# Performance work log

Hardware: AMD Instinct MI355X
Metric: run time of the kernel (lower is better)

Reference implementation:

```python
import jax, jax.numpy as jnp
import numpy as np

N = 4096      # n_patches / nodes
IN_FEAT = 512
EMBED = 512
HEADS = 8
HEAD_DIM = EMBED // HEADS
SCALING = HEAD_DIM ** -0.5


def setup_inputs() -> dict:
    key = jax.random.key(0)
    ks = jax.random.split(key, 7)
    x = jax.random.normal(ks[0], (N, IN_FEAT), dtype=jnp.float32)
    adj = jax.random.randint(ks[1], (N, N), 0, 2, dtype=jnp.int32)
    s = 0.04  # ~xavier scale for 512x512
    WQ = jax.random.normal(ks[2], (EMBED, IN_FEAT), dtype=jnp.float32) * s
    WK = jax.random.normal(ks[3], (EMBED, IN_FEAT), dtype=jnp.float32) * s
    WV = jax.random.normal(ks[4], (EMBED, IN_FEAT), dtype=jnp.float32) * s
    we = jax.random.normal(ks[5], (1, HEAD_DIM), dtype=jnp.float32) * 0.1
    be = jnp.zeros((1,), dtype=jnp.float32)
    return {"x": x, "adj": adj, "WQ": WQ, "WK": WK, "WV": WV, "we": we, "be": be}


def reference(x, adj, WQ, WK, WV, we, be):
    n = x.shape[0]
    # projections: [N, E] -> [H, N, head_dim]
    Q = (x @ WQ.T).reshape(n, HEADS, HEAD_DIM).transpose(1, 0, 2)
    K = (x @ WK.T).reshape(n, HEADS, HEAD_DIM).transpose(1, 0, 2)
    V = (x @ WV.T).reshape(n, HEADS, HEAD_DIM).transpose(1, 0, 2)
    # scores + per-query energy term: [H, N, N]
    energy = Q @ we.T + be                      # [H, N, 1]
    attn = jnp.einsum('hqd,hkd->hqk', Q, K) * SCALING + energy
    # adjacency mask (broadcast over heads)
    attn = attn + jnp.where(adj > 0, 0.0, -jnp.inf)
    attn = jax.nn.softmax(attn, axis=-1)
    # winner-take-all: one-hot at row max, divided by num_heads
    hard = (attn == jnp.max(attn, axis=-1, keepdims=True)).astype(jnp.float32) / HEADS
    out = jnp.einsum('hqk,hkd->hqd', hard, V)   # [H, N, head_dim]
    return out.transpose(1, 0, 2).reshape(n, EMBED)
```

## Files before the change

### kernel.cpp

```cpp
#include <hip/hip_runtime.h>
#include <hip/hip_bf16.h>
#include <float.h>
#include <stdint.h>

#define NPT    4096
#define EMB    512
#define NH     8
#define HD     64
#define KSPLIT 32

typedef __attribute__((ext_vector_type(8))) short bf16x8;
typedef __attribute__((ext_vector_type(4))) float f32x4;
typedef uint32_t u32;

__device__ __forceinline__ void async_ld16(const void* gsrc, void* ldst) {
    __builtin_amdgcn_global_load_lds(
        (const __attribute__((address_space(1))) u32*)gsrc,
        (__attribute__((address_space(3))) u32*)ldst, 16, 0, 0);
}

__device__ __forceinline__ void split3(float a, unsigned short& h,
                                       unsigned short& m, unsigned short& l) {
    __hip_bfloat16 bh = __float2bfloat16(a);
    float fh = __bfloat162float(bh);
    float r1 = a - fh;
    __hip_bfloat16 bm = __float2bfloat16(r1);
    float fm = __bfloat162float(bm);
    float r2 = r1 - fm;
    __hip_bfloat16 bl = __float2bfloat16(r2);
    h = *reinterpret_cast<unsigned short*>(&bh);
    m = *reinterpret_cast<unsigned short*>(&bm);
    l = *reinterpret_cast<unsigned short*>(&bl);
}

__global__ __launch_bounds__(256) void prep_kernel(const float* __restrict__ x,
                                                   const float* __restrict__ wq,
                                                   const float* __restrict__ wk,
                                                   const float* __restrict__ wv,
                                                   const int* __restrict__ adj,
                                                   unsigned short* __restrict__ xs,
                                                   unsigned short* __restrict__ wqs,
                                                   unsigned short* __restrict__ wks,
                                                   unsigned short* __restrict__ wvs,
                                                   unsigned* __restrict__ bits_t) {
    int y = blockIdx.y;
    size_t i = (size_t)blockIdx.x * 256 + threadIdx.x;
    if (y == 4) {
        int q = (int)(i >> 7), w = (int)i & 127;
        const int4* p = (const int4*)(adj + (size_t)q * NPT + w * 32);
        unsigned m = 0;
#pragma unroll
        for (int j = 0; j < 8; ++j) {
            int4 v = p[j];
            m |= (v.x != 0 ? 1u : 0u) << (j * 4 + 0);
            m |= (v.y != 0 ? 1u : 0u) << (j * 4 + 1);
            m |= (v.z != 0 ? 1u : 0u) << (j * 4 + 2);
            m |= (v.w != 0 ? 1u : 0u) << (j * 4 + 3);
        }
        bits_t[(size_t)w * NPT + q] = m;
    } else if (y == 0) {
        const size_t PL = (size_t)NPT * EMB;
        float4 v = ((const float4*)x)[i];
        ushort4 h, m, l;
        split3(v.x, h.x, m.x, l.x);
        split3(v.y, h.y, m.y, l.y);
        split3(v.z, h.z, m.z, l.z);
        split3(v.w, h.w, m.w, l.w);
        ((ushort4*)xs)[i]            = h;
        ((ushort4*)(xs + PL))[i]     = m;
        ((ushort4*)(xs + 2 * PL))[i] = l;
    } else {
        const size_t WPL = 262144;
        if (i >= WPL / 4) return;
        const float* src = (y == 1) ? wq : (y == 2) ? wk : wv;
        unsigned short* dst = (y == 1) ? wqs : (y == 2) ? wks : wvs;
        float4 v = ((const float4*)src)[i];
        int e  = (int)(i >> 7);
        int k0 = ((int)i & 127) * 4;
        int ebk = e >> 6, el = e & 63;
        int kc = k0 >> 5, g = (k0 >> 3) & 3, dd = k0 & 7;
        size_t off = ((((size_t)ebk * 16 + kc) * 4 + g) * 64 + el) * 8 + dd;
        ushort4 h, m, l;
        split3(v.x, h.x, m.x, l.x);
        split3(v.y, h.y, m.y, l.y);
        split3(v.z, h.z, m.z, l.z);
        split3(v.w, h.w, m.w, l.w);
        *(ushort4*)(dst + off)           = h;
        *(ushort4*)(dst + WPL + off)     = m;
        *(ushort4*)(dst + 2 * WPL + off) = l;
    }
}

__global__ __launch_bounds__(256) void gemm_mfma(const unsigned short* __restrict__ xs,
                                                 const unsigned short* __restrict__ wqs,
                                                 const unsigned short* __restrict__ wks,
                                                 const unsigned short* __restrict__ wvs,
                                                 unsigned short* __restrict__ Q3,
                                                 unsigned short* __restrict__ K3,
                                                 float* __restrict__ V) {
    const int z = blockIdx.z;
    const unsigned short* W3 = (z == 0) ? wqs : (z == 1) ? wks : wvs;
    const size_t XPL = (size_t)NPT * EMB;
    const size_t WPL = 262144;
    const size_t OPL = (size_t)NH * NPT * HD;

    const int nb = blockIdx.x * 128;
    const int ebk = blockIdx.y;
    const int tid = threadIdx.x;
    const int wv = tid >> 6, lane = tid & 63;
    const int m = lane & 15, quad = lane >> 4;
    const int n0 = nb + wv * 32;

    __shared__ __align__(16) unsigned short Ws[2][3 * 2048];

    auto prefetchW = [&](int kc, int buf) {
#pragma unroll
        for (int i2 = 0; i2 < 3; ++i2) {
            int c = wv + 4 * i2;
            int p = c >> 2, sub = c & 3;
            const unsigned short* src = W3 + (size_t)p * WPL
                + ((size_t)ebk * 16 + kc) * 2048 + (sub * 64 + lane) * 8;
            async_ld16(src, &Ws[buf][p * 2048 + sub * 512]);
        }
    };
    bf16x8 bfA[2][3], bfB[2][3];
    auto load_bf = [&](bf16x8 (&bf)[2][3], int kc) {
#pragma unroll
        for (int nt = 0; nt < 2; ++nt)
#pragma unroll
            for (int p = 0; p < 3; ++p)
                bf[nt][p] = *(const bf16x8*)(xs + (size_t)p * XPL
                    + (size_t)(n0 + nt * 16 + m) * EMB + kc * 32 + quad * 8);
    };

    f32x4 acc[4][2];
#pragma unroll
    for (int mt = 0; mt < 4; ++mt)
#pragma unroll
        for (int nt = 0; nt < 2; ++nt) acc[mt][nt] = (f32x4){0.f, 0.f, 0.f, 0.f};

    prefetchW(0, 0);
    load_bf(bfA, 0);

    auto iter = [&](int kc, int buf, bf16x8 (&cur)[2][3], bf16x8 (&nxt)[2][3]) {
        __syncthreads();
        if (kc < 15) { prefetchW(kc + 1, buf ^ 1); load_bf(nxt, kc + 1); }
#pragma unroll
        for (int ga = 0; ga < 3; ++ga) {
            bf16x8 af[4];
#pragma unroll
            for (int mt = 0; mt < 4; ++mt)
                af[mt] = *(const bf16x8*)&Ws[buf][ga * 2048 + (quad * 64 + mt * 16 + m) * 8];
#pragma unroll
            for (int pb = 0; pb < 3 - ga; ++pb)
#pragma unroll
                for (int mt = 0; mt < 4; ++mt)
#pragma unroll
                    for (int nt = 0; nt < 2; ++nt)
                        acc[mt][nt] = __builtin_amdgcn_mfma_f32_16x16x32_bf16(
                            af[mt], cur[nt][pb], acc[mt][nt], 0, 0, 0);
        }
    };

#pragma unroll 1
    for (int kc2 = 0; kc2 < 16; kc2 += 2) {
        iter(kc2, 0, bfA, bfB);
        iter(kc2 + 1, 1, bfB, bfA);
    }

    const int h = ebk;
#pragma unroll
    for (int mt = 0; mt < 4; ++mt)
#pragma unroll
        for (int nt = 0; nt < 2; ++nt) {
            const int n = n0 + nt * 16 + m;
            const int d0 = mt * 16 + quad * 4;
            f32x4 a = acc[mt][nt];
            if (z == 2) {
                *(f32x4*)(V + (size_t)n * EMB + ebk * 64 + d0) = a;
            } else {
                ushort4 ph, pm, pl;
                split3(a[0], ph.x, pm.x, pl.x);
                split3(a[1], ph.y, pm.y, pl.y);
                split3(a[2], ph.z, pm.z, pl.z);
                split3(a[3], ph.w, pm.w, pl.w);
                unsigned short* O3 = (z == 0) ? Q3 : K3;
                size_t off = ((size_t)h * 128 + (n >> 5)) * 2048
                           + (d0 >> 3) * 256 + (n & 31) * 8 + (d0 & 7);
                *(ushort4*)(O3 + off)           = ph;
                *(ushort4*)(O3 + OPL + off)     = pm;
                *(ushort4*)(O3 + 2 * OPL + off) = pl;
            }
        }
}

__global__ __launch_bounds__(256) void score_mfma(const unsigned short* __restrict__ Q3,
                                                  const unsigned short* __restrict__ K3,
                                                  const unsigned* __restrict__ bits_t,
                                                  float* __restrict__ pval,
                                                  int* __restrict__ pidx) {
    const int qb = blockIdx.x * 128;
    const int ks = blockIdx.y;
    const int tid = threadIdx.x;
    const int wv = tid >> 6, lane = tid & 63;
    const int m = lane & 15, quad = lane >> 4;
    const size_t PL = (size_t)NH * NPT * HD;
    const int kq = qb + wv * 32;

    __shared__ __align__(16) unsigned short Ks[3][3 * 2048];

    auto prefetchK = [&](int t) {
        int h = t >> 2, kt = ks * 4 + (t & 3), buf = t % 3;
#pragma unroll
        for (int i2 = 0; i2 < 3; ++i2) {
            int c = wv + 4 * i2;
            int p = c >> 2, sub = c & 3;
            const unsigned short* src = K3 + (size_t)p * PL
                + ((size_t)h * 128 + kt) * 2048 + (sub * 64 + lane) * 8;
            async_ld16(src, &Ks[buf][p * 2048 + sub * 512]);
        }
    };

    prefetchK(0);
    prefetchK(1);

    bf16x8 qf[2][2][3];
    float bestv[2]; int besti[2];

#pragma unroll 1
    for (int t = 0; t < NH * 4; ++t) {
        const int h = t >> 2, kst = t & 3, buf = t % 3;
        const int kbase = ks * 128 + kst * 32;

        asm volatile("s_waitcnt vmcnt(3)\n\ts_barrier" ::: "memory");

        if (kst == 0) {
#pragma unroll
            for (int nt = 0; nt < 2; ++nt)
#pragma unroll
                for (int dc = 0; dc < 2; ++dc)
#pragma unroll
                    for (int p = 0; p < 3; ++p)
                        qf[nt][dc][p] = *(const bf16x8*)(Q3 + (size_t)p * PL
                            + ((size_t)h * 128 + (kq >> 5)) * 2048
                            + (dc * 4 + quad) * 256 + (nt * 16 + m) * 8);
            bestv[0] = bestv[1] = -FLT_MAX;
            besti[0] = besti[1] = 0;
        }

        unsigned bw[2];
#pragma unroll
        for (int nt = 0; nt < 2; ++nt)
            bw[nt] = bits_t[(size_t)(ks * 4 + kst) * NPT + kq + nt * 16 + m];

        if (t + 2 < NH * 4) prefetchK(t + 2);

        f32x4 acc[2][2];
#pragma unroll
        for (int mt = 0; mt < 2; ++mt)
#pragma unroll
            for (int nt = 0; nt < 2; ++nt) acc[mt][nt] = (f32x4){0.f, 0.f, 0.f, 0.f};

#pragma unroll
        for (int ga = 0; ga < 3; ++ga) {
            bf16x8 kf[2][2];
#pragma unroll
            for (int mt = 0; mt < 2; ++mt)
#pragma unroll
                for (int dc = 0; dc < 2; ++dc)
                    kf[mt][dc] = *(const bf16x8*)
                        &Ks[buf][ga * 2048 + ((dc * 4 + quad) * 32 + mt * 16 + m) * 8];
#pragma unroll
            for (int pb = 0; pb < 3 - ga; ++pb)
#pragma unroll
                for (int dc = 0; dc < 2; ++dc)
#pragma unroll
                    for (int mt = 0; mt < 2; ++mt)
#pragma unroll
                        for (int nt = 0; nt < 2; ++nt)
                            acc[mt][nt] = __builtin_amdgcn_mfma_f32_16x16x32_bf16(
                                kf[mt][dc], qf[nt][dc][pb], acc[mt][nt], 0, 0, 0);
        }

#pragma unroll
        for (int nt = 0; nt < 2; ++nt) {
            unsigned w = bw[nt];
#pragma unroll
            for (int mt = 0; mt < 2; ++mt) {
                int k0 = mt * 16 + quad * 4;
                f32x4 a = acc[mt][nt];
#pragma unroll
                for (int r = 0; r < 4; ++r) {
                    if ((w >> (k0 + r)) & 1u) {
                        float s = a[r];
                        if (s > bestv[nt]) { bestv[nt] = s; besti[nt] = kbase + k0 + r; }
                    }
                }
            }
        }

        if (kst == 3) {
#pragma unroll
            for (int nt = 0; nt < 2; ++nt) {
                float v = bestv[nt]; int bi = besti[nt];
#pragma unroll
                for (int off = 16; off < 64; off <<= 1) {
                    float ov = __shfl_xor(v, off);
                    int   oi = __shfl_xor(bi, off);
                    if (ov > v || (ov == v && oi < bi)) { v = ov; bi = oi; }
                }
                if (quad == 0) {
                    size_t o = ((size_t)h * KSPLIT + ks) * NPT + kq + nt * 16 + m;
                    pval[o] = v; pidx[o] = bi;
                }
            }
        }
    }
}

__global__ __launch_bounds__(128) void gather_out(const float* __restrict__ V,
                                                  const float* __restrict__ pval,
                                                  const int* __restrict__ pidx,
                                                  float* __restrict__ out) {
    const int q = blockIdx.x;
    const int tid = threadIdx.x;
    __shared__ int widx[NH];
    if (tid < NH) {
        float bv = -FLT_MAX; int bi = 0;
        for (int ks = 0; ks < KSPLIT; ++ks) {
            size_t off = ((size_t)tid * KSPLIT + ks) * NPT + q;
            float v = pval[off];
            if (v > bv) { bv = v; bi = pidx[off]; }
        }
        widx[tid] = bi;
    }
    __syncthreads();
    const int h = tid >> 4;
    const int d4 = (tid & 15) * 4;
    const int k = widx[h];
    float4 v = *(const float4*)(V + (size_t)k * EMB + h * HD + d4);
    v.x *= 0.125f; v.y *= 0.125f; v.z *= 0.125f; v.w *= 0.125f;
    *(float4*)(out + (size_t)q * EMB + h * HD + d4) = v;
}

extern "C" void kernel_launch(void* const* d_in, const int* in_sizes, int n_in,
                              void* d_out, int out_size, void* d_ws, size_t ws_size,
                              hipStream_t stream) {
    const float* x   = (const float*)d_in[0];
    const int*   adj = (const int*)d_in[1];
    const float* WQ  = (const float*)d_in[2];
    const float* WK  = (const float*)d_in[3];
    const float* WV  = (const float*)d_in[4];
    float* out = (float*)d_out;

    char* ws = (char*)d_ws;
    const size_t HMB = 512u * 1024;
    unsigned short* xs   = (unsigned short*)(ws);
    unsigned short* wqs  = (unsigned short*)(ws + 24 * HMB);
    unsigned short* wks  = (unsigned short*)(ws + 27 * HMB);
    unsigned short* wvs  = (unsigned short*)(ws + 30 * HMB);
    unsigned short* Q3   = (unsigned short*)(ws + 33 * HMB);
    unsigned short* K3   = (unsigned short*)(ws + 57 * HMB);
    float*          V    = (float*)(ws + 81 * HMB);
    unsigned*       bits = (unsigned*)(ws + 97 * HMB);
    float*          pval = (float*)(ws);
    int*            pidx = (int*)(ws + 8 * HMB);

    prep_kernel<<<dim3(2048, 5), dim3(256), 0, stream>>>(x, WQ, WK, WV, adj,
                                                         xs, wqs, wks, wvs, bits);
    gemm_mfma<<<dim3(NPT / 128, NH, 3), dim3(256), 0, stream>>>(xs, wqs, wks, wvs, Q3, K3, V);
    score_mfma<<<dim3(NPT / 128, KSPLIT), dim3(256), 0, stream>>>(Q3, K3, bits, pval, pidx);
    gather_out<<<dim3(NPT), dim3(128), 0, stream>>>(V, pval, pidx, out);
}
```

Measured before the change: 276.2 us.

## Fuse Q/K/V projections into one GEMM block with tiled x layout

The projection GEMM now computes Q, K and V in a single block, so each loaded x fragment is reused across all three weight matrices instead of being reloaded by three separate z-blocks. The prep kernel writes x in a tiled 16-row by 32-column layout so the GEMM's fragment loads become contiguous. Warps are arranged 2x2 over n and e, and the grid shrinks from 768 to 256 blocks. The double-buffered prefetch is dropped in favour of a single buffer with two barriers per k-step, which exposes load latency and leaves fewer blocks per CU, while the 24 accumulator tiles per thread raise register pressure.

```diff
diff --git a/kernel.cpp b/kernel.cpp
--- a/kernel.cpp
+++ b/kernel.cpp
@@ -61,14 +61,18 @@
     } else if (y == 0) {
         const size_t PL = (size_t)NPT * EMB;
         float4 v = ((const float4*)x)[i];
+        int n  = (int)(i >> 7);
+        int k0 = ((int)i & 127) * 4;
+        int kc = k0 >> 5, kg = (k0 >> 3) & 3, dd = k0 & 7;
+        size_t off = ((((size_t)(n >> 4) * 16 + kc) * 4 + kg) * 16 + (n & 15)) * 8 + dd;
         ushort4 h, m, l;
         split3(v.x, h.x, m.x, l.x);
         split3(v.y, h.y, m.y, l.y);
         split3(v.z, h.z, m.z, l.z);
         split3(v.w, h.w, m.w, l.w);
-        ((ushort4*)xs)[i]            = h;
-        ((ushort4*)(xs + PL))[i]     = m;
-        ((ushort4*)(xs + 2 * PL))[i] = l;
+        *(ushort4*)(xs + off)          = h;
+        *(ushort4*)(xs + PL + off)     = m;
+        *(ushort4*)(xs + 2 * PL + off) = l;
     } else {
         const size_t WPL = 262144;
         if (i >= WPL / 4) return;
@@ -98,100 +102,100 @@
                                                  unsigned short* __restrict__ Q3,
                                                  unsigned short* __restrict__ K3,
                                                  float* __restrict__ V) {
-    const int z = blockIdx.z;
-    const unsigned short* W3 = (z == 0) ? wqs : (z == 1) ? wks : wvs;
     const size_t XPL = (size_t)NPT * EMB;
     const size_t WPL = 262144;
     const size_t OPL = (size_t)NH * NPT * HD;
 
-    const int nb = blockIdx.x * 128;
+    const int tn  = blockIdx.x;
     const int ebk = blockIdx.y;
     const int tid = threadIdx.x;
     const int wv = tid >> 6, lane = tid & 63;
+    const int wn = wv & 1, we = wv >> 1;
     const int m = lane & 15, quad = lane >> 4;
-    const int n0 = nb + wv * 32;
-
-    __shared__ __align__(16) unsigned short Ws[2][3 * 2048];
-
-    auto prefetchW = [&](int kc, int buf) {
-#pragma unroll
-        for (int i2 = 0; i2 < 3; ++i2) {
+    const int n0 = tn * 128 + wn * 64;
+    const int e0 = we * 32;
+
+    __shared__ __align__(16) unsigned short Ws[3 * 3 * 4 * 64 * 8];
+
+    const unsigned short* Wz[3] = {wqs, wks, wvs};
+
+    f32x4 acc[3][2][4];
+#pragma unroll
+    for (int z = 0; z < 3; ++z)
+#pragma unroll
+        for (int mt = 0; mt < 2; ++mt)
+#pragma unroll
+            for (int nt = 0; nt < 4; ++nt) acc[z][mt][nt] = (f32x4){0.f, 0.f, 0.f, 0.f};
+
+#pragma unroll 1
+    for (int kc = 0; kc < 16; ++kc) {
+        __syncthreads();
+#pragma unroll
+        for (int i2 = 0; i2 < 9; ++i2) {
             int c = wv + 4 * i2;
-            int p = c >> 2, sub = c & 3;
-            const unsigned short* src = W3 + (size_t)p * WPL
-                + ((size_t)ebk * 16 + kc) * 2048 + (sub * 64 + lane) * 8;
-            async_ld16(src, &Ws[buf][p * 2048 + sub * 512]);
-        }
-    };
-    bf16x8 bfA[2][3], bfB[2][3];
-    auto load_bf = [&](bf16x8 (&bf)[2][3], int kc) {
-#pragma unroll
-        for (int nt = 0; nt < 2; ++nt)
+            int z = c / 12, p = (c / 4) % 3, kg = c & 3;
+            const unsigned short* src = Wz[z] + (size_t)p * WPL
+                + (((size_t)ebk * 16 + kc) * 4 + kg) * 512 + lane * 8;
+            async_ld16(src, &Ws[((z * 3 + p) * 4 + kg) * 512]);
+        }
+        bf16x8 xf[4][3];
+#pragma unroll
+        for (int nt = 0; nt < 4; ++nt) {
+            int tni = tn * 8 + wn * 4 + nt;
 #pragma unroll
             for (int p = 0; p < 3; ++p)
-                bf[nt][p] = *(const bf16x8*)(xs + (size_t)p * XPL
-                    + (size_t)(n0 + nt * 16 + m) * EMB + kc * 32 + quad * 8);
-    };
-
-    f32x4 acc[4][2];
-#pragma unroll
-    for (int mt = 0; mt < 4; ++mt)
-#pragma unroll
-        for (int nt = 0; nt < 2; ++nt) acc[mt][nt] = (f32x4){0.f, 0.f, 0.f, 0.f};
-
-    prefetchW(0, 0);
-    load_bf(bfA, 0);
-
-    auto iter = [&](int kc, int buf, bf16x8 (&cur)[2][3], bf16x8 (&nxt)[2][3]) {
+                xf[nt][p] = *(const bf16x8*)(xs + (size_t)p * XPL
+                    + ((((size_t)tni * 16 + kc) * 4 + quad) * 16 + m) * 8);
+        }
         __syncthreads();
-        if (kc < 15) { prefetchW(kc + 1, buf ^ 1); load_bf(nxt, kc + 1); }
+
 #pragma unroll
         for (int ga = 0; ga < 3; ++ga) {
-            bf16x8 af[4];
-#pragma unroll
-            for (int mt = 0; mt < 4; ++mt)
-                af[mt] = *(const bf16x8*)&Ws[buf][ga * 2048 + (quad * 64 + mt * 16 + m) * 8];
-#pragma unroll
-            for (int pb = 0; pb < 3 - ga; ++pb)
-#pragma unroll
-                for (int mt = 0; mt < 4; ++mt)
-#pragma unroll
-                    for (int nt = 0; nt < 2; ++nt)
-                        acc[mt][nt] = __builtin_amdgcn_mfma_f32_16x16x32_bf16(
-                            af[mt], cur[nt][pb], acc[mt][nt], 0, 0, 0);
-        }
-    };
-
-#pragma unroll 1
-    for (int kc2 = 0; kc2 < 16; kc2 += 2) {
-        iter(kc2, 0, bfA, bfB);
-        iter(kc2 + 1, 1, bfB, bfA);
+#pragma unroll
+            for (int z = 0; z < 3; ++z) {
+                bf16x8 af[2];
+#pragma unroll
+                for (int mt = 0; mt < 2; ++mt)
+                    af[mt] = *(const bf16x8*)
+                        &Ws[(((z * 3 + ga) * 4 + quad) * 64 + e0 + mt * 16 + m) * 8];
+#pragma unroll
+                for (int pb = 0; pb < 3 - ga; ++pb)
+#pragma unroll
+                    for (int mt = 0; mt < 2; ++mt)
+#pragma unroll
+                        for (int nt = 0; nt < 4; ++nt)
+                            acc[z][mt][nt] = __builtin_amdgcn_mfma_f32_16x16x32_bf16(
+                                af[mt], xf[nt][pb], acc[z][mt][nt], 0, 0, 0);
+            }
+        }
     }
 
     const int h = ebk;
 #pragma unroll
-    for (int mt = 0; mt < 4; ++mt)
-#pragma unroll
-        for (int nt = 0; nt < 2; ++nt) {
-            const int n = n0 + nt * 16 + m;
-            const int d0 = mt * 16 + quad * 4;
-            f32x4 a = acc[mt][nt];
-            if (z == 2) {
-                *(f32x4*)(V + (size_t)n * EMB + ebk * 64 + d0) = a;
-            } else {
-                ushort4 ph, pm, pl;
-                split3(a[0], ph.x, pm.x, pl.x);
-                split3(a[1], ph.y, pm.y, pl.y);
-                split3(a[2], ph.z, pm.z, pl.z);
-                split3(a[3], ph.w, pm.w, pl.w);
-                unsigned short* O3 = (z == 0) ? Q3 : K3;
-                size_t off = ((size_t)h * 128 + (n >> 5)) * 2048
-                           + (d0 >> 3) * 256 + (n & 31) * 8 + (d0 & 7);
-                *(ushort4*)(O3 + off)           = ph;
-                *(ushort4*)(O3 + OPL + off)     = pm;
-                *(ushort4*)(O3 + 2 * OPL + off) = pl;
+    for (int z = 0; z < 3; ++z)
+#pragma unroll
+        for (int mt = 0; mt < 2; ++mt)
+#pragma unroll
+            for (int nt = 0; nt < 4; ++nt) {
+                const int n = n0 + nt * 16 + m;
+                const int dL = e0 + mt * 16 + quad * 4;
+                f32x4 a = acc[z][mt][nt];
+                if (z == 2) {
+                    *(f32x4*)(V + (size_t)n * EMB + ebk * 64 + dL) = a;
+                } else {
+                    ushort4 ph, pm, pl;
+                    split3(a[0], ph.x, pm.x, pl.x);
+                    split3(a[1], ph.y, pm.y, pl.y);
+                    split3(a[2], ph.z, pm.z, pl.z);
+                    split3(a[3], ph.w, pm.w, pl.w);
+                    unsigned short* O3 = (z == 0) ? Q3 : K3;
+                    size_t off = ((size_t)h * 128 + (n >> 5)) * 2048
+                               + (dL >> 3) * 256 + (n & 31) * 8 + (dL & 7);
+                    *(ushort4*)(O3 + off)           = ph;
+                    *(ushort4*)(O3 + OPL + off)     = pm;
+                    *(ushort4*)(O3 + 2 * OPL + off) = pl;
+                }
             }
-        }
 }
 
 __global__ __launch_bounds__(256) void score_mfma(const unsigned short* __restrict__ Q3,
@@ -368,7 +372,7 @@
 
     prep_kernel<<<dim3(2048, 5), dim3(256), 0, stream>>>(x, WQ, WK, WV, adj,
                                                          xs, wqs, wks, wvs, bits);
-    gemm_mfma<<<dim3(NPT / 128, NH, 3), dim3(256), 0, stream>>>(xs, wqs, wks, wvs, Q3, K3, V);
+    gemm_mfma<<<dim3(32, NH), dim3(256), 0, stream>>>(xs, wqs, wks, wvs, Q3, K3, V);
     score_mfma<<<dim3(NPT / 128, KSPLIT), dim3(256), 0, stream>>>(Q3, K3, bits, pval, pidx);
     gather_out<<<dim3(NPT), dim3(128), 0, stream>>>(V, pval, pidx, out);
 }
```

After: 278.8 us. No clear change (+0.9%).
